# Kernel tuning notes

Hardware: AMD Instinct MI355X
Metric: run time of the kernel (lower is better)

## Reference

```python
import jax, jax.numpy as jnp
import numpy as np

N_NODES = 100000
N_EDGES = 1600000
NFEAT, NHID, NCLASS = 256, 128, 64


def gcn_conv(x, edge_index, edge_weight, W):
    # PyG GCNConv (normalize=False, add_self_loops=False, bias=False):
    # h = x @ W.T; out[i] = sum over edges (j->i) of w_e * h[j]
    h = x @ W.T                                   # [N, out]
    src, dst = edge_index[0], edge_index[1]
    msgs = h[src] * edge_weight[:, None]          # [E, out]
    return jax.ops.segment_sum(msgs, dst, num_segments=x.shape[0])


def setup_inputs() -> dict:
    key = jax.random.key(0)
    ks = jax.random.split(key, 7)
    x = jax.random.normal(ks[0], (N_NODES, NFEAT), dtype=jnp.float32)
    edge_index1 = jax.random.randint(ks[1], (2, N_EDGES), 0, N_NODES, dtype=jnp.int64)
    edge_index2 = jax.random.randint(ks[2], (2, N_EDGES), 0, N_NODES, dtype=jnp.int64)
    edge_weight1 = jax.random.uniform(ks[3], (N_EDGES,), dtype=jnp.float32)
    edge_weight2 = jax.random.uniform(ks[4], (N_EDGES,), dtype=jnp.float32)
    W1 = jax.random.normal(ks[5], (NHID, NFEAT), dtype=jnp.float32) * (1.0 / np.sqrt(NFEAT))
    W2 = jax.random.normal(ks[6], (NCLASS, NHID), dtype=jnp.float32) * (1.0 / np.sqrt(NHID))
    return {"x": x, "edge_index1": edge_index1, "edge_index2": edge_index2,
            "edge_weight1": edge_weight1, "edge_weight2": edge_weight2,
            "W1": W1, "W2": W2}


def reference(x, edge_index1, edge_index2, edge_weight1, edge_weight2, W1, W2):
    h = jax.nn.relu(gcn_conv(x, edge_index1, edge_weight1, W1))
    out = gcn_conv(h, edge_index2, edge_weight2, W2)
    return out
```

## Files before the change

### kernel.cpp

```cpp
#include <hip/hip_runtime.h>

typedef __attribute__((ext_vector_type(8))) short short8;
typedef __attribute__((ext_vector_type(4))) float floatx4;

#define BKT_SHIFT 7
#define BKT_MASK 127
#define CAP 2560

__device__ __forceinline__ ushort f2bf(float f) {
    uint u = __builtin_bit_cast(uint, f);
    uint r = (u + 0x7FFFu + ((u >> 16) & 1u)) >> 16;
    return (ushort)r;
}
__device__ __forceinline__ float bflo(uint h) {
    return __builtin_bit_cast(float, h << 16);
}
__device__ __forceinline__ float bfhi(uint h) {
    return __builtin_bit_cast(float, h & 0xffff0000u);
}

__global__ __launch_bounds__(256) void prep(const uint* __restrict__ ei,
                                            int* __restrict__ flag,
                                            const float* __restrict__ W1,
                                            const float* __restrict__ W2,
                                            ushort* __restrict__ w1b,
                                            ushort* __restrict__ w2b,
                                            int* __restrict__ cntz,
                                            int n1, int n2) {
    if (blockIdx.x == 0 && threadIdx.x < 64) {
        uint v = ei[2 * threadIdx.x + 1];
        unsigned long long b = __ballot(v != 0u);
        if (threadIdx.x == 0) *flag = (b == 0ull) ? 1 : 0;
    }
    int i = blockIdx.x * 256 + threadIdx.x;
    if (i < 2048) cntz[i] = 0;
    if (i < n1) w1b[i] = f2bf(W1[i]);
    else if (i < n1 + n2) w2b[i - n1] = f2bf(W2[i - n1]);
}

__global__ __launch_bounds__(256) void cvt_x(const float* __restrict__ X,
                                             ushort* __restrict__ XB, long n) {
    long i = ((long)blockIdx.x * 256 + threadIdx.x) * 8;
    if (i < n) {
        floatx4 a = *(const floatx4*)(X + i);
        floatx4 b = *(const floatx4*)(X + i + 4);
        short8 o;
        #pragma unroll
        for (int j = 0; j < 4; j++) {
            o[j]     = (short)f2bf(a[j]);
            o[4 + j] = (short)f2bf(b[j]);
        }
        *(short8*)(XB + i) = o;
    }
}

template<int K, int NOUT>
__global__ __launch_bounds__(256) void gemm_bt(const ushort* __restrict__ Xb,
                                               const ushort* __restrict__ W,
                                               ushort* __restrict__ Y, int N) {
    constexpr int NT = NOUT / 16;
    constexpr int KS = K / 32;
    constexpr int ROWS = 64;
    constexpr int RB = K * 2;
    constexpr int LPR = RB / 16;
    constexpr int RPI = 64 / LPR;
    constexpr int NI = 16 / RPI;
    __shared__ __align__(16) char xs[ROWS * RB];

    const int tid  = threadIdx.x;
    const int lane = tid & 63;
    const int wv   = tid >> 6;
    const int t    = lane & 15;
    const int q    = lane >> 4;
    const int rbase = blockIdx.x * ROWS;

    #pragma unroll
    for (int i = 0; i < NI; i++) {
        int rl0 = wv * 16 + i * RPI;
        int grow0 = rbase + rl0;
        if (grow0 < N) {
            int rl = rl0 + lane / LPR;
            const char* src = (const char*)Xb + (long)grow0 * RB + (lane / LPR) * RB
                            + (((lane % LPR) * 16) ^ ((rl & 7) << 5));
            __builtin_amdgcn_global_load_lds(
                (const __attribute__((address_space(1))) void*)src,
                (__attribute__((address_space(3))) void*)&xs[rl0 * RB], 16, 0, 0);
        }
    }
    __syncthreads();

    floatx4 acc[NT];
    #pragma unroll
    for (int b = 0; b < NT; b++)
        #pragma unroll
        for (int i = 0; i < 4; i++) acc[b][i] = 0.f;

    const int lrow = wv * 16 + t;
    const char* xrow = &xs[lrow * RB];
    const uint swz = (uint)((t & 7) << 5);

    for (int ks = 0; ks < KS; ks++) {
        short8 af = *(const short8*)(xrow + (((uint)(ks * 64 + q * 16)) ^ swz));
        #pragma unroll
        for (int nt = 0; nt < NT; nt++) {
            short8 bf = *(const short8*)(W + (long)(nt * 16 + t) * K + ks * 32 + q * 8);
            acc[nt] = __builtin_amdgcn_mfma_f32_16x16x32_bf16(af, bf, acc[nt], 0, 0, 0);
        }
    }

    const int obase = rbase + wv * 16;
    #pragma unroll
    for (int j = 0; j < 4; j++) {
        int orow = obase + q * 4 + j;
        if (orow < N) {
            #pragma unroll
            for (int nt = 0; nt < NT; nt++)
                Y[(long)orow * NOUT + nt * 16 + t] = f2bf(acc[nt][j]);
        }
    }
}

__global__ __launch_bounds__(256) void bin_edges(const void* __restrict__ eidx,
                                                 const float* __restrict__ ew,
                                                 int* __restrict__ cntg,
                                                 int2* __restrict__ binA, int E, int nbk,
                                                 const int* __restrict__ flag) {
    __shared__ int lc[1024], lb[1024], lo[1024];
    for (int t = threadIdx.x; t < 1024; t += 256) { lc[t] = 0; lo[t] = 0; }
    __syncthreads();
    int S = (E + gridDim.x - 1) / gridDim.x;
    int s = blockIdx.x * S, e = min(E, s + S);
    bool f = *flag;
    for (int i = s + threadIdx.x; i < e; i += 256) {
        int dst = f ? (int)((const long long*)eidx)[i + E] : ((const int*)eidx)[i + E];
        atomicAdd(&lc[dst >> BKT_SHIFT], 1);
    }
    __syncthreads();
    for (int t = threadIdx.x; t < nbk; t += 256)
        lb[t] = lc[t] ? atomicAdd(&cntg[t], lc[t]) : 0;
    __syncthreads();
    for (int i = s + threadIdx.x; i < e; i += 256) {
        int src, dst;
        if (f) { const long long* p = (const long long*)eidx; src = (int)p[i]; dst = (int)p[i + E]; }
        else   { const int* p = (const int*)eidx;             src = p[i];      dst = p[i + E]; }
        int bk = dst >> BKT_SHIFT;
        int pos = lb[bk] + atomicAdd(&lo[bk], 1);
        if (pos < CAP)
            binA[(long)bk * CAP + pos] = make_int2(src | ((dst & BKT_MASK) << 24),
                                                   __builtin_bit_cast(int, ew[i]));
    }
}

__global__ __launch_bounds__(256) void sort_bucket(const int2* __restrict__ binA,
                                                   const int* __restrict__ cntg,
                                                   int2* __restrict__ pairs,
                                                   int2* __restrict__ rr, int N) {
    __shared__ int hcnt[128], hcur[128];
    __shared__ int2 ps[CAP];
    int b = blockIdx.x, t = threadIdx.x;
    const long base = (long)b * CAP;
    int n = min(cntg[b], CAP);
    if (t < 128) { hcnt[t] = 0; hcur[t] = 0; }
    __syncthreads();
    for (int i = t; i < n; i += 256)
        atomicAdd(&hcnt[(uint)binA[base + i].x >> 24], 1);
    __syncthreads();
    for (int off = 1; off < 128; off <<= 1) {
        int v = (t >= off && t < 128) ? hcnt[t - off] : 0;
        __syncthreads();
        if (t < 128) hcnt[t] += v;
        __syncthreads();
    }
    if (t < 128) {
        int node = (b << BKT_SHIFT) + t;
        int ex = t ? hcnt[t - 1] : 0;
        if (node < N) rr[node] = make_int2((int)base + ex, (int)base + hcnt[t]);
    }
    __syncthreads();
    for (int i = t; i < n; i += 256) {
        int2 p = binA[base + i];
        int dl = (uint)p.x >> 24;
        int pos = (dl ? hcnt[dl - 1] : 0) + atomicAdd(&hcur[dl], 1);
        ps[pos] = make_int2(p.x & 0x00FFFFFF, p.y);
    }
    __syncthreads();
    for (int j = t; j < n; j += 256) pairs[base + j] = ps[j];
}

template<int F, bool RELU, bool BF16OUT>
__global__ __launch_bounds__(256) void gather_nodes(const ushort* __restrict__ H,
                                                    const int2* __restrict__ pairs,
                                                    const int2* __restrict__ rr,
                                                    void* __restrict__ out, int N) {
    constexpr int LPE = F / 4;
    constexpr int G   = 64 / LPE;
    constexpr int U   = 4;
    int wave = (blockIdx.x * 256 + threadIdx.x) >> 6;
    int lane = threadIdx.x & 63;
    int node = wave;
    if (node >= N) return;
    const int g  = lane / LPE;
    const int cL = lane % LPE;
    int2 se = rr[node];
    int s = se.x, e = se.y;

    float a0 = 0.f, a1 = 0.f, a2 = 0.f, a3 = 0.f;
    float b0 = 0.f, b1 = 0.f, b2 = 0.f, b3 = 0.f;
    float c0 = 0.f, c1 = 0.f, c2 = 0.f, c3 = 0.f;
    float d0 = 0.f, d1 = 0.f, d2 = 0.f, d3 = 0.f;

    int cnt = e - s;
    int full = cnt / (G * U);
    for (int k = 0; k < full; k++) {
        int idx = s + k * U * G + g;
        int2 p0 = pairs[idx];
        int2 p1 = pairs[idx + G];
        int2 p2 = pairs[idx + 2 * G];
        int2 p3 = pairs[idx + 3 * G];
        uint2 h0 = *(const uint2*)(H + (long)p0.x * F + 4 * cL);
        uint2 h1 = *(const uint2*)(H + (long)p1.x * F + 4 * cL);
        uint2 h2 = *(const uint2*)(H + (long)p2.x * F + 4 * cL);
        uint2 h3 = *(const uint2*)(H + (long)p3.x * F + 4 * cL);
        float w0 = __builtin_bit_cast(float, p0.y), w1 = __builtin_bit_cast(float, p1.y);
        float w2 = __builtin_bit_cast(float, p2.y), w3 = __builtin_bit_cast(float, p3.y);
        a0 += w0 * bflo(h0.x);  a1 += w0 * bfhi(h0.x);
        a2 += w0 * bflo(h0.y);  a3 += w0 * bfhi(h0.y);
        b0 += w1 * bflo(h1.x);  b1 += w1 * bfhi(h1.x);
        b2 += w1 * bflo(h1.y);  b3 += w1 * bfhi(h1.y);
        c0 += w2 * bflo(h2.x);  c1 += w2 * bfhi(h2.x);
        c2 += w2 * bflo(h2.y);  c3 += w2 * bfhi(h2.y);
        d0 += w3 * bflo(h3.x);  d1 += w3 * bfhi(h3.x);
        d2 += w3 * bflo(h3.y);  d3 += w3 * bfhi(h3.y);
    }
    for (int idx = s + full * U * G + g; idx < e; idx += G) {
        int2 p = pairs[idx];
        uint2 h = *(const uint2*)(H + (long)p.x * F + 4 * cL);
        float w = __builtin_bit_cast(float, p.y);
        a0 += w * bflo(h.x);  a1 += w * bfhi(h.x);
        a2 += w * bflo(h.y);  a3 += w * bfhi(h.y);
    }
    float r0 = (a0 + b0) + (c0 + d0);
    float r1 = (a1 + b1) + (c1 + d1);
    float r2 = (a2 + b2) + (c2 + d2);
    float r3 = (a3 + b3) + (c3 + d3);
    #pragma unroll
    for (int m = LPE; m < 64; m <<= 1) {
        r0 += __shfl_xor(r0, m);
        r1 += __shfl_xor(r1, m);
        r2 += __shfl_xor(r2, m);
        r3 += __shfl_xor(r3, m);
    }
    if (g == 0) {
        if (BF16OUT) {
            if (RELU) {
                r0 = fmaxf(r0, 0.f); r1 = fmaxf(r1, 0.f);
                r2 = fmaxf(r2, 0.f); r3 = fmaxf(r3, 0.f);
            }
            uint2 pk;
            pk.x = (uint)f2bf(r0) | ((uint)f2bf(r1) << 16);
            pk.y = (uint)f2bf(r2) | ((uint)f2bf(r3) << 16);
            *(uint2*)((uint*)out + (long)node * (F / 2) + 2 * cL) = pk;
        } else {
            float4 r; r.x = r0; r.y = r1; r.z = r2; r.w = r3;
            *(float4*)((float*)out + (long)node * F + 4 * cL) = r;
        }
    }
}

extern "C" void kernel_launch(void* const* d_in, const int* in_sizes, int n_in,
                              void* d_out, int out_size, void* d_ws, size_t ws_size,
                              hipStream_t stream) {
    const float* x   = (const float*)d_in[0];
    const void*  ei1 = d_in[1];
    const void*  ei2 = d_in[2];
    const float* ew1 = (const float*)d_in[3];
    const float* ew2 = (const float*)d_in[4];
    const float* W1  = (const float*)d_in[5];
    const float* W2  = (const float*)d_in[6];

    const int N = in_sizes[0] / 256;
    const int E = in_sizes[3];
    const int NBK = (N + BKT_MASK) >> BKT_SHIFT;

    char* ws = (char*)d_ws;
    size_t off = 0;
    ushort* XW     = (ushort*)(ws + off); off += (size_t)N * 128 * 2;
    ushort* hbuf   = (ushort*)(ws + off); off += (size_t)N * 128 * 2;
    int2*   binA   = (int2*)  (ws + off); off += (size_t)NBK * CAP * 8;
    int2*   pairs  = (int2*)  (ws + off); off += (size_t)NBK * CAP * 8;
    int2*   rr     = (int2*)  (ws + off); off += (size_t)N * 8;
    int*    cnt1   = (int*)   (ws + off); off += 1024 * 4;
    int*    cnt2   = (int*)   (ws + off); off += 1024 * 4;
    ushort* w1b    = (ushort*)(ws + off); off += 128 * 256 * 2;
    ushort* w2b    = (ushort*)(ws + off); off += 64 * 128 * 2;
    int*    flag   = (int*)   (ws + off);
    ushort* XB     = hbuf;
    ushort* H2     = XW;

    prep<<<160, 256, 0, stream>>>((const uint*)ei1, flag, W1, W2, w1b, w2b,
                                  cnt1, 128 * 256, 64 * 128);
    cvt_x<<<(int)(((long)N * 256 / 8 + 255) / 256), 256, 0, stream>>>(x, XB, (long)N * 256);

    int gblocks = (N + 63) / 64;
    gemm_bt<256, 128><<<gblocks, 256, 0, stream>>>(XB, w1b, XW, N);

    bin_edges<<<256, 256, 0, stream>>>(ei1, ew1, cnt1, binA, E, NBK, flag);
    sort_bucket<<<NBK, 256, 0, stream>>>(binA, cnt1, pairs, rr, N);
    gather_nodes<128, true, true><<<(N + 3) / 4, 256, 0, stream>>>(
        XW, pairs, rr, hbuf, N);

    gemm_bt<128, 64><<<gblocks, 256, 0, stream>>>(hbuf, w2b, H2, N);
    bin_edges<<<256, 256, 0, stream>>>(ei2, ew2, cnt2, binA, E, NBK, flag);
    sort_bucket<<<NBK, 256, 0, stream>>>(binA, cnt2, pairs, rr, N);
    gather_nodes<64, false, false><<<(N + 3) / 4, 256, 0, stream>>>(
        H2, pairs, rr, (float*)d_out, N);
}
```

Baseline: 507.0 us.

## Merge independent pipeline stages into shared multi-role kernel launches

Independent stages now share a launch through block-index dispatch: x conversion with layer-1 edge binning, GEMM with bucket sorting, and layer-1 gather with layer-2 binning. This cuts the launch count and lets work that does not depend on each other run side by side on the GPU. When the workspace is too small, a fallback path reads fp32 x straight into the GEMM and converts it in registers. The cost is larger shared-memory allocations per block, which can lower occupancy for the GEMM blocks. Correctness also relies on binA being free for reuse once the layer-1 sort has finished.

```diff
diff --git a/kernel.cpp b/kernel.cpp
--- a/kernel.cpp
+++ b/kernel.cpp
@@ -38,9 +38,10 @@
     else if (i < n1 + n2) w2b[i - n1] = f2bf(W2[i - n1]);
 }
 
-__global__ __launch_bounds__(256) void cvt_x(const float* __restrict__ X,
-                                             ushort* __restrict__ XB, long n) {
-    long i = ((long)blockIdx.x * 256 + threadIdx.x) * 8;
+
+__device__ __forceinline__ void dev_cvt(const float* __restrict__ X,
+                                        ushort* __restrict__ XB, long n, int bid) {
+    long i = ((long)bid * 256 + threadIdx.x) * 8;
     if (i < n) {
         floatx4 a = *(const floatx4*)(X + i);
         floatx4 b = *(const floatx4*)(X + i + 4);
@@ -54,82 +55,18 @@
     }
 }
 
-template<int K, int NOUT>
-__global__ __launch_bounds__(256) void gemm_bt(const ushort* __restrict__ Xb,
-                                               const ushort* __restrict__ W,
-                                               ushort* __restrict__ Y, int N) {
-    constexpr int NT = NOUT / 16;
-    constexpr int KS = K / 32;
-    constexpr int ROWS = 64;
-    constexpr int RB = K * 2;
-    constexpr int LPR = RB / 16;
-    constexpr int RPI = 64 / LPR;
-    constexpr int NI = 16 / RPI;
-    __shared__ __align__(16) char xs[ROWS * RB];
-
-    const int tid  = threadIdx.x;
-    const int lane = tid & 63;
-    const int wv   = tid >> 6;
-    const int t    = lane & 15;
-    const int q    = lane >> 4;
-    const int rbase = blockIdx.x * ROWS;
-
-    #pragma unroll
-    for (int i = 0; i < NI; i++) {
-        int rl0 = wv * 16 + i * RPI;
-        int grow0 = rbase + rl0;
-        if (grow0 < N) {
-            int rl = rl0 + lane / LPR;
-            const char* src = (const char*)Xb + (long)grow0 * RB + (lane / LPR) * RB
-                            + (((lane % LPR) * 16) ^ ((rl & 7) << 5));
-            __builtin_amdgcn_global_load_lds(
-                (const __attribute__((address_space(1))) void*)src,
-                (__attribute__((address_space(3))) void*)&xs[rl0 * RB], 16, 0, 0);
-        }
-    }
-    __syncthreads();
-
-    floatx4 acc[NT];
-    #pragma unroll
-    for (int b = 0; b < NT; b++)
-        #pragma unroll
-        for (int i = 0; i < 4; i++) acc[b][i] = 0.f;
-
-    const int lrow = wv * 16 + t;
-    const char* xrow = &xs[lrow * RB];
-    const uint swz = (uint)((t & 7) << 5);
-
-    for (int ks = 0; ks < KS; ks++) {
-        short8 af = *(const short8*)(xrow + (((uint)(ks * 64 + q * 16)) ^ swz));
-        #pragma unroll
-        for (int nt = 0; nt < NT; nt++) {
-            short8 bf = *(const short8*)(W + (long)(nt * 16 + t) * K + ks * 32 + q * 8);
-            acc[nt] = __builtin_amdgcn_mfma_f32_16x16x32_bf16(af, bf, acc[nt], 0, 0, 0);
-        }
-    }
-
-    const int obase = rbase + wv * 16;
-    #pragma unroll
-    for (int j = 0; j < 4; j++) {
-        int orow = obase + q * 4 + j;
-        if (orow < N) {
-            #pragma unroll
-            for (int nt = 0; nt < NT; nt++)
-                Y[(long)orow * NOUT + nt * 16 + t] = f2bf(acc[nt][j]);
-        }
-    }
-}
-
-__global__ __launch_bounds__(256) void bin_edges(const void* __restrict__ eidx,
-                                                 const float* __restrict__ ew,
-                                                 int* __restrict__ cntg,
-                                                 int2* __restrict__ binA, int E, int nbk,
-                                                 const int* __restrict__ flag) {
-    __shared__ int lc[1024], lb[1024], lo[1024];
+__device__ __forceinline__ void dev_bin(int* sm, const void* __restrict__ eidx,
+                                        const float* __restrict__ ew,
+                                        int* __restrict__ cntg, int2* __restrict__ binA,
+                                        int E, int nbk, int nblk, int bid,
+                                        const int* __restrict__ flag) {
+    int* lc = sm;
+    int* lb = sm + 1024;
+    int* lo = sm + 2048;
     for (int t = threadIdx.x; t < 1024; t += 256) { lc[t] = 0; lo[t] = 0; }
     __syncthreads();
-    int S = (E + gridDim.x - 1) / gridDim.x;
-    int s = blockIdx.x * S, e = min(E, s + S);
+    int S = (E + nblk - 1) / nblk;
+    int s = bid * S, e = min(E, s + S);
     bool f = *flag;
     for (int i = s + threadIdx.x; i < e; i += 256) {
         int dst = f ? (int)((const long long*)eidx)[i + E] : ((const int*)eidx)[i + E];
@@ -151,13 +88,14 @@
     }
 }
 
-__global__ __launch_bounds__(256) void sort_bucket(const int2* __restrict__ binA,
-                                                   const int* __restrict__ cntg,
-                                                   int2* __restrict__ pairs,
-                                                   int2* __restrict__ rr, int N) {
-    __shared__ int hcnt[128], hcur[128];
-    __shared__ int2 ps[CAP];
-    int b = blockIdx.x, t = threadIdx.x;
+__device__ __forceinline__ void dev_sort(char* smem, const int2* __restrict__ binA,
+                                         const int* __restrict__ cntg,
+                                         int2* __restrict__ pairs,
+                                         int2* __restrict__ rr, int N, int b) {
+    int* hcnt = (int*)smem;
+    int* hcur = hcnt + 128;
+    int2* ps  = (int2*)(smem + 1024);
+    int t = threadIdx.x;
     const long base = (long)b * CAP;
     int n = min(cntg[b], CAP);
     if (t < 128) { hcnt[t] = 0; hcur[t] = 0; }
@@ -187,15 +125,106 @@
     for (int j = t; j < n; j += 256) pairs[base + j] = ps[j];
 }
 
+template<int K, int NOUT, bool XF32>
+__device__ __forceinline__ void dev_gemm(char* xs, const void* __restrict__ Xv,
+                                         const ushort* __restrict__ W,
+                                         ushort* __restrict__ Y, int N, int bid) {
+    constexpr int NT = NOUT / 16;
+    constexpr int KS = K / 32;
+    constexpr int RB = XF32 ? K * 4 : K * 2;
+    const int tid  = threadIdx.x;
+    const int lane = tid & 63;
+    const int wv   = tid >> 6;
+    const int t    = lane & 15;
+    const int q    = lane >> 4;
+    const int rbase = bid * 64;
+
+    if (XF32) {
+        #pragma unroll
+        for (int i = 0; i < 16; i++) {
+            int rl = wv * 16 + i;
+            int grow = rbase + rl;
+            if (grow < N) {
+                const char* src = (const char*)Xv + (long)grow * RB
+                                + ((lane * 16) ^ ((rl & 7) << 5));
+                __builtin_amdgcn_global_load_lds(
+                    (const __attribute__((address_space(1))) void*)src,
+                    (__attribute__((address_space(3))) void*)&xs[rl * RB], 16, 0, 0);
+            }
+        }
+    } else {
+        constexpr int LPR = RB / 16;
+        constexpr int RPI = 64 / LPR;
+        constexpr int NI = 16 / RPI;
+        #pragma unroll
+        for (int i = 0; i < NI; i++) {
+            int rl0 = wv * 16 + i * RPI;
+            int grow0 = rbase + rl0;
+            if (grow0 < N) {
+                int rl = rl0 + lane / LPR;
+                const char* src = (const char*)Xv + (long)grow0 * RB + (lane / LPR) * RB
+                                + (((lane % LPR) * 16) ^ ((rl & 7) << 5));
+                __builtin_amdgcn_global_load_lds(
+                    (const __attribute__((address_space(1))) void*)src,
+                    (__attribute__((address_space(3))) void*)&xs[rl0 * RB], 16, 0, 0);
+            }
+        }
+    }
+    __syncthreads();
+
+    floatx4 acc[NT];
+    #pragma unroll
+    for (int b = 0; b < NT; b++)
+        #pragma unroll
+        for (int i = 0; i < 4; i++) acc[b][i] = 0.f;
+
+    const int lrow = wv * 16 + t;
+    const char* xrow = &xs[lrow * RB];
+    const uint swz = (uint)((t & 7) << 5);
+
+    for (int ks = 0; ks < KS; ks++) {
+        short8 af;
+        if (XF32) {
+            uint off = ((uint)(ks * 128 + q * 32)) ^ swz;
+            floatx4 lo = *(const floatx4*)(xrow + off);
+            floatx4 hi = *(const floatx4*)(xrow + off + 16);
+            #pragma unroll
+            for (int j = 0; j < 4; j++) {
+                af[j]     = (short)f2bf(lo[j]);
+                af[4 + j] = (short)f2bf(hi[j]);
+            }
+        } else {
+            af = *(const short8*)(xrow + (((uint)(ks * 64 + q * 16)) ^ swz));
+        }
+        #pragma unroll
+        for (int nt = 0; nt < NT; nt++) {
+            short8 bf = *(const short8*)(W + (long)(nt * 16 + t) * K + ks * 32 + q * 8);
+            acc[nt] = __builtin_amdgcn_mfma_f32_16x16x32_bf16(af, bf, acc[nt], 0, 0, 0);
+        }
+    }
+
+    const int obase = rbase + wv * 16;
+    #pragma unroll
+    for (int j = 0; j < 4; j++) {
+        int orow = obase + q * 4 + j;
+        if (orow < N) {
+            #pragma unroll
+            for (int nt = 0; nt < NT; nt++)
+                Y[(long)orow * NOUT + nt * 16 + t] = f2bf(acc[nt][j]);
+        }
+    }
+}
+
 template<int F, bool RELU, bool BF16OUT>
-__global__ __launch_bounds__(256) void gather_nodes(const ushort* __restrict__ H,
-                                                    const int2* __restrict__ pairs,
-                                                    const int2* __restrict__ rr,
-                                                    void* __restrict__ out, int N) {
+__device__ __forceinline__ void dev_gather(const ushort* __restrict__ H,
+                                           const int2* __restrict__ pairs,
+                                           const int2* __restrict__ rr,
+                                           void* __restrict__ out, int N, int bid) {
+    constexpr int L   = F / 2;
     constexpr int LPE = F / 4;
     constexpr int G   = 64 / LPE;
     constexpr int U   = 4;
-    int wave = (blockIdx.x * 256 + threadIdx.x) >> 6;
+    int wave = (bid * 256 + (int)threadIdx.x) >> 6;
     int lane = threadIdx.x & 63;
     int node = wave;
     if (node >= N) return;
@@ -259,12 +288,68 @@
             uint2 pk;
             pk.x = (uint)f2bf(r0) | ((uint)f2bf(r1) << 16);
             pk.y = (uint)f2bf(r2) | ((uint)f2bf(r3) << 16);
-            *(uint2*)((uint*)out + (long)node * (F / 2) + 2 * cL) = pk;
+            *(uint2*)((uint*)out + (long)node * L + 2 * cL) = pk;
         } else {
             float4 r; r.x = r0; r.y = r1; r.z = r2; r.w = r3;
             *(float4*)((float*)out + (long)node * F + 4 * cL) = r;
         }
     }
+}
+
+
+__global__ __launch_bounds__(256) void fuse_cvt_bin(const float* __restrict__ X,
+                                                    ushort* __restrict__ XB, long n,
+                                                    const void* __restrict__ eidx,
+                                                    const float* __restrict__ ew,
+                                                    int* __restrict__ cntg,
+                                                    int2* __restrict__ binA, int E, int nbk,
+                                                    const int* __restrict__ flag) {
+    __shared__ __align__(16) int sm[3072];
+    if (blockIdx.x < 256) dev_bin(sm, eidx, ew, cntg, binA, E, nbk, 256, blockIdx.x, flag);
+    else dev_cvt(X, XB, n, blockIdx.x - 256);
+}
+
+__global__ __launch_bounds__(256) void bin_only(const void* __restrict__ eidx,
+                                                const float* __restrict__ ew,
+                                                int* __restrict__ cntg,
+                                                int2* __restrict__ binA, int E, int nbk,
+                                                const int* __restrict__ flag) {
+    __shared__ __align__(16) int sm[3072];
+    dev_bin(sm, eidx, ew, cntg, binA, E, nbk, (int)gridDim.x, blockIdx.x, flag);
+}
+
+template<int K, int NOUT, bool XF32>
+__global__ __launch_bounds__(256) void fuse_gemm_sort(const void* __restrict__ Xv,
+                                                      const ushort* __restrict__ W,
+                                                      ushort* __restrict__ Y, int N, int gb,
+                                                      const int2* __restrict__ binA,
+                                                      const int* __restrict__ cntg,
+                                                      int2* __restrict__ pairs,
+                                                      int2* __restrict__ rr) {
+    constexpr int RB = XF32 ? K * 4 : K * 2;
+    constexpr int GS = 64 * RB;
+    constexpr int SS = 1024 + CAP * 8;
+    constexpr int SM = GS > SS ? GS : SS;
+    __shared__ __align__(16) char smem[SM];
+    if ((int)blockIdx.x < gb) dev_gemm<K, NOUT, XF32>(smem, Xv, W, Y, N, blockIdx.x);
+    else dev_sort(smem, binA, cntg, pairs, rr, N, blockIdx.x - gb);
+}
+
+template<int F, bool RELU, bool BF16OUT>
+__global__ __launch_bounds__(256) void fuse_gather_bin(const ushort* __restrict__ H,
+                                                       const int2* __restrict__ pairs,
+                                                       const int2* __restrict__ rr,
+                                                       void* __restrict__ out, int N,
+                                                       const void* __restrict__ eidx,
+                                                       const float* __restrict__ ew,
+                                                       int* __restrict__ cntg,
+                                                       int2* __restrict__ binA, int E, int nbk,
+                                                       const int* __restrict__ flag, int binblk) {
+    __shared__ __align__(16) int sm[3072];
+    if ((int)blockIdx.x < binblk)
+        dev_bin(sm, eidx, ew, cntg, binA, E, nbk, binblk, blockIdx.x, flag);
+    else
+        dev_gather<F, RELU, BF16OUT>(H, pairs, rr, out, N, blockIdx.x - binblk);
 }
 
 extern "C" void kernel_launch(void* const* d_in, const int* in_sizes, int n_in,
@@ -282,36 +367,54 @@
     const int E = in_sizes[3];
     const int NBK = (N + BKT_MASK) >> BKT_SHIFT;
 
+    const size_t SZ_F   = (size_t)N * 128 * 2;
+    const size_t SZ_XB  = (size_t)N * 256 * 2;
+    const size_t SZ_BIN = (size_t)NBK * CAP * 8;
+    const size_t SZ_TAIL = (size_t)N * 8 + 2 * 4096 + 128 * 256 * 2 + 64 * 128 * 2 + 256;
+    const bool bfp = ws_size >= SZ_F + SZ_XB + 2 * SZ_BIN + SZ_TAIL;
+
     char* ws = (char*)d_ws;
     size_t off = 0;
-    ushort* XW     = (ushort*)(ws + off); off += (size_t)N * 128 * 2;
-    ushort* hbuf   = (ushort*)(ws + off); off += (size_t)N * 128 * 2;
-    int2*   binA   = (int2*)  (ws + off); off += (size_t)NBK * CAP * 8;
-    int2*   pairs  = (int2*)  (ws + off); off += (size_t)NBK * CAP * 8;
-    int2*   rr     = (int2*)  (ws + off); off += (size_t)N * 8;
-    int*    cnt1   = (int*)   (ws + off); off += 1024 * 4;
-    int*    cnt2   = (int*)   (ws + off); off += 1024 * 4;
-    ushort* w1b    = (ushort*)(ws + off); off += 128 * 256 * 2;
-    ushort* w2b    = (ushort*)(ws + off); off += 64 * 128 * 2;
-    int*    flag   = (int*)   (ws + off);
-    ushort* XB     = hbuf;
-    ushort* H2     = XW;
+    ushort* XW = (ushort*)(ws + off); off += SZ_F;
+    ushort* XB = nullptr;
+    ushort* hbuf;
+    if (bfp) { XB = (ushort*)(ws + off); hbuf = XB; off += SZ_XB; }
+    else     { hbuf = (ushort*)(ws + off); off += SZ_F; }
+    int2* binA  = (int2*)(ws + off); off += SZ_BIN;
+    int2* pairs = (int2*)(ws + off); off += SZ_BIN;
+    int2* rr    = (int2*)(ws + off); off += (size_t)N * 8;
+    int*  cnt1  = (int*) (ws + off); off += 4096;
+    int*  cnt2  = (int*) (ws + off); off += 4096;
+    ushort* w1b = (ushort*)(ws + off); off += 128 * 256 * 2;
+    ushort* w2b = (ushort*)(ws + off); off += 64 * 128 * 2;
+    int*  flag  = (int*) (ws + off);
+    ushort* H2  = XW;
+
+    const int gb = (N + 63) / 64;
+    const int gab = (N + 3) / 4;
 
     prep<<<160, 256, 0, stream>>>((const uint*)ei1, flag, W1, W2, w1b, w2b,
                                   cnt1, 128 * 256, 64 * 128);
-    cvt_x<<<(int)(((long)N * 256 / 8 + 255) / 256), 256, 0, stream>>>(x, XB, (long)N * 256);
-
-    int gblocks = (N + 63) / 64;
-    gemm_bt<256, 128><<<gblocks, 256, 0, stream>>>(XB, w1b, XW, N);
-
-    bin_edges<<<256, 256, 0, stream>>>(ei1, ew1, cnt1, binA, E, NBK, flag);
-    sort_bucket<<<NBK, 256, 0, stream>>>(binA, cnt1, pairs, rr, N);
-    gather_nodes<128, true, true><<<(N + 3) / 4, 256, 0, stream>>>(
-        XW, pairs, rr, hbuf, N);
-
-    gemm_bt<128, 64><<<gblocks, 256, 0, stream>>>(hbuf, w2b, H2, N);
-    bin_edges<<<256, 256, 0, stream>>>(ei2, ew2, cnt2, binA, E, NBK, flag);
-    sort_bucket<<<NBK, 256, 0, stream>>>(binA, cnt2, pairs, rr, N);
-    gather_nodes<64, false, false><<<(N + 3) / 4, 256, 0, stream>>>(
-        H2, pairs, rr, (float*)d_out, N);
-}
+
+    if (bfp) {
+        long n = (long)N * 256;
+        int cvb = (int)((n / 8 + 255) / 256);
+        fuse_cvt_bin<<<256 + cvb, 256, 0, stream>>>(x, XB, n, ei1, ew1, cnt1,
+                                                    binA, E, NBK, flag);
+        fuse_gemm_sort<256, 128, false><<<gb + NBK, 256, 0, stream>>>(
+            XB, w1b, XW, N, gb, binA, cnt1, pairs, rr);
+    } else {
+        bin_only<<<256, 256, 0, stream>>>(ei1, ew1, cnt1, binA, E, NBK, flag);
+        fuse_gemm_sort<256, 128, true><<<gb + NBK, 256, 0, stream>>>(
+            x, w1b, XW, N, gb, binA, cnt1, pairs, rr);
+    }
+
+    fuse_gather_bin<128, true, true><<<256 + gab, 256, 0, stream>>>(
+        XW, pairs, rr, hbuf, N, ei2, ew2, cnt2, binA, E, NBK, flag, 256);
+
+    fuse_gemm_sort<128, 64, false><<<gb + NBK, 256, 0, stream>>>(
+        hbuf, w2b, H2, N, gb, binA, cnt2, pairs, rr);
+
+    fuse_gather_bin<64, false, false><<<gab, 256, 0, stream>>>(
+        H2, pairs, rr, d_out, N, ei2, ew2, cnt2, binA, E, NBK, flag, 0);
+}
```

New measurement: 472.0 us. 1.07x faster.
